# Optimization experiments

Hardware: AMD Instinct MI355X
Metric: run time of the kernel (lower is better)

The kernel has to match this reference:

```python
import jax, jax.numpy as jnp
import numpy as np

H_DIM = 64
GRID = 8
NBR = 2.0
BN_EPS = 1e-5
N_SEQ = 64
N_PED = 64
BOTTLENECK = 1024


def setup_inputs() -> dict:
    key = jax.random.key(0)
    k0, k1, k2, k3 = jax.random.split(key, 4)
    batch = N_SEQ * N_PED
    h_states = jax.random.normal(k0, (1, batch, H_DIM), jnp.float32)
    # positions spread over a 4x4 area so some neighbors fall inside the 2.0 neighborhood
    end_pos = jax.random.uniform(k1, (batch, 2), jnp.float32) * 4.0
    rel_pos = jax.random.normal(k2, (batch, 2), jnp.float32)
    starts = jnp.arange(N_SEQ, dtype=jnp.int32) * N_PED
    seq_start_end = jnp.stack([starts, starts + N_PED], axis=1)
    in_dim = GRID * GRID * H_DIM  # 4096
    W = jax.random.normal(k3, (in_dim, BOTTLENECK), jnp.float32) / np.sqrt(in_dim)
    b = jnp.zeros((BOTTLENECK,), jnp.float32)
    gamma = jnp.ones((BOTTLENECK,), jnp.float32)
    beta = jnp.zeros((BOTTLENECK,), jnp.float32)
    return {"h_states": h_states, "seq_start_end": seq_start_end, "end_pos": end_pos,
            "rel_pos": rel_pos, "W": W, "b": b, "gamma": gamma, "beta": beta}


def _pool_scene(hidden, pos):
    # hidden: (n, h), pos: (n, 2). Pair (i, j): ped j binned into ped i's grid.
    n, h = hidden.shape
    g2 = GRID * GRID
    half = NBR / 2.0
    tl_x = pos[:, 0] - half
    tl_y = pos[:, 1] + half
    br_x = pos[:, 0] + half
    br_y = pos[:, 1] - half
    px = pos[None, :, 0]  # (1, n) -> broadcast over i
    py = pos[None, :, 1]
    cell_x = jnp.floor((px - tl_x[:, None]) / NBR * GRID)
    cell_y = jnp.floor((tl_y[:, None] - py) / NBR * GRID)
    grid = (cell_x + cell_y * GRID).astype(jnp.int32) + 1  # slot 0 = trash bin
    oob = ((px >= br_x[:, None]) | (px <= tl_x[:, None]) |
           (py >= tl_y[:, None]) | (py <= br_y[:, None]) |
           jnp.eye(n, dtype=bool))  # self-interaction excluded
    grid = grid + (jnp.arange(n, dtype=jnp.int32) * g2)[:, None]
    grid = jnp.where(oob, 0, grid)  # (n, n)
    src = jnp.broadcast_to(hidden[None], (n, n, h)).reshape(-1, h)
    buf = jnp.zeros((n * g2 + 1, h), hidden.dtype).at[grid.reshape(-1)].add(src)
    return buf[1:].reshape(n, g2 * h)


def reference(h_states, seq_start_end, end_pos, rel_pos, W, b, gamma, beta):
    batch = end_pos.shape[0]
    n_seq = seq_start_end.shape[0]
    n_ped = batch // n_seq  # equal-length scenes by construction
    hid = h_states.reshape(-1, H_DIM).reshape(n_seq, n_ped, H_DIM)
    pos = end_pos.reshape(n_seq, n_ped, 2)
    pool_h = jax.vmap(_pool_scene)(hid, pos).reshape(batch, -1)  # (batch, 4096)
    x = pool_h @ W + b
    # BatchNorm1d in training mode (batch statistics, biased variance)
    mean = jnp.mean(x, axis=0)
    var = jnp.var(x, axis=0)
    x = (x - mean) * jax.lax.rsqrt(var + BN_EPS) * gamma + beta
    return jax.nn.relu(x)
```

## Files before the change

kernel.cpp:

```cpp
#include <hip/hip_runtime.h>
#include <hip/hip_bf16.h>


#define NPED  64
#define BATCH 4096
#define HDIM  64
#define G2    64
#define KDIM  4096
#define NOUT  1024

typedef __attribute__((ext_vector_type(8))) short short8;
typedef __attribute__((ext_vector_type(4))) float f32x4;

__device__ __forceinline__ unsigned short f2bf(float f) {
    __hip_bfloat16 h = __float2bfloat16(f);
    return *reinterpret_cast<unsigned short*>(&h);
}

__device__ __forceinline__ void lds_load16(const void* g, void* l) {
    __builtin_amdgcn_global_load_lds(
        (const __attribute__((address_space(1))) void*)g,
        (__attribute__((address_space(3))) void*)l, 16, 0, 0);
}

__global__ __launch_bounds__(512) void pool_kernel(const float* __restrict__ h,
                                                   const float* __restrict__ pos,
                                                   unsigned short* __restrict__ A2) {
    __shared__ float hs[NPED * HDIM];
    __shared__ float pl[NPED * 2];
    int t = threadIdx.x;
    int w = t >> 6, lane = t & 63;
    int p0 = blockIdx.x * 8;
    int sbase = p0 & ~(NPED - 1);
    if (t < 128) pl[t] = pos[sbase * 2 + t];
    {
        const float4* src = (const float4*)(h + (size_t)sbase * HDIM);
        float4* dst = (float4*)hs;
        dst[t] = src[t];
        dst[t + 512] = src[t + 512];
    }
    __syncthreads();

    int i = p0 + w;
    int il = i & (NPED - 1);
    float cx0 = pl[2 * il], cy0 = pl[2 * il + 1];
    float tlx = cx0 - 1.f, tly = cy0 + 1.f, brx = cx0 + 1.f, bry = cy0 - 1.f;
    float px = pl[2 * lane], py = pl[2 * lane + 1];
    bool inb = (lane != il) && !(px >= brx || px <= tlx || py >= tly || py <= bry);
    int cellx = (int)floorf((px - tlx) * 4.f);
    int celly = (int)floorf((tly - py) * 4.f);
    int cell = cellx + celly * 8;
    inb = inb && ((unsigned)cell < 64u);

    int mtile = i >> 4, r = i & 15;
    unsigned short* outb = A2 + (size_t)mtile * 65536 + r * 8
                              + (lane >> 5) * 512 + ((lane >> 3) & 3) * 128 + (lane & 7);
    const float* hrow = hs + lane;
    #pragma unroll
    for (int c = 0; c < 64; ++c) {
        unsigned long long m = __ballot(inb && (cell == c));
        float a = 0.f;
        while (m) {
            int j = __builtin_ctzll(m);
            m &= m - 1;
            a += hrow[j * HDIM];
        }
        outb[c * 1024] = f2bf(a);
    }
}

__global__ __launch_bounds__(256) void wt_kernel(const float* __restrict__ W,
                                                 unsigned short* __restrict__ Wt,
                                                 float* __restrict__ stats) {
    __shared__ unsigned short tile[64][66];
    int k0 = blockIdx.x * 64;
    int n0 = blockIdx.y * 64;
    int t = threadIdx.x;
    if (blockIdx.x == 0 && blockIdx.y < 8) stats[blockIdx.y * 256 + t] = 0.f;
    #pragma unroll
    for (int p = 0; p < 4; ++p) {
        int lin = p * 256 + t;
        int c4 = lin & 15, kl = lin >> 4;
        float4 v = ((const float4*)(W + (size_t)(k0 + kl) * NOUT + n0))[c4];
        tile[c4 * 4 + 0][kl] = f2bf(v.x);
        tile[c4 * 4 + 1][kl] = f2bf(v.y);
        tile[c4 * 4 + 2][kl] = f2bf(v.z);
        tile[c4 * 4 + 3][kl] = f2bf(v.w);
    }
    __syncthreads();
    unsigned int* out = (unsigned int*)Wt;
    #pragma unroll
    for (int p = 0; p < 8; ++p) {
        int lin = p * 256 + t;
        int ku = lin & 31, nl = lin >> 5;
        unsigned int v = (unsigned int)tile[nl][2 * ku] |
                         ((unsigned int)tile[nl][2 * ku + 1] << 16);
        out[(size_t)(n0 + nl) * (KDIM / 2) + (k0 >> 1) + ku] = v;
    }
}


__global__ __launch_bounds__(512, 2) void gemm_kernel(const unsigned short* __restrict__ A2,
                                                      const unsigned short* __restrict__ Bt,
                                                      float* __restrict__ C,
                                                      float* __restrict__ stats) {
    __shared__ __align__(16) char shmem[65536];
    unsigned short* Bs = (unsigned short*)shmem;

    int t = threadIdx.x;
    int w = t >> 6, lane = t & 63;
    int kh = w >> 2, wsub = w & 3;

    int bid = blockIdx.x;
    int yb = bid & 7, xb = bid >> 3;
    int m0 = xb * 128, n0 = yb * 128;
    int wm = (wsub >> 1) * 64, wn = (wsub & 1) * 64;

    const unsigned short* Ab = A2 + (size_t)((m0 >> 4) + (wm >> 4)) * 65536 + lane * 8;
    const unsigned short* Wtb = Bt + (size_t)n0 * KDIM;

    int kh_t = t >> 8, tt = t & 255;

    f32x4 acc[4][4];
    #pragma unroll
    for (int i = 0; i < 4; ++i)
        #pragma unroll
        for (int j = 0; j < 4; ++j)
            acc[i][j] = (f32x4){0.f, 0.f, 0.f, 0.f};

    for (int sk = 0; sk < 32; ++sk) {
        #pragma unroll
        for (int q = 0; q < 4; ++q) {
            int s = q * 256 + tt;
            int row = s >> 3;
            int swz = (s & 7) ^ (row & 7);
            lds_load16(Wtb + (size_t)row * KDIM + kh_t * 2048 + sk * 64 + swz * 8,
                       Bs + kh_t * 8192 + s * 8);
        }
        short8 af[2][4];
        #pragma unroll
        for (int kk = 0; kk < 2; ++kk)
            #pragma unroll
            for (int i = 0; i < 4; ++i)
                af[kk][i] = *(const short8*)(Ab + (size_t)i * 65536 +
                                             (size_t)(kh * 64 + sk * 2 + kk) * 512);
        __syncthreads();
        const unsigned short* Bsr = Bs + kh * 8192;
        #pragma unroll
        for (int kk = 0; kk < 2; ++kk) {
            #pragma unroll
            for (int j = 0; j < 4; ++j) {
                int rB = wn + j * 16 + (lane & 15);
                short8 b = *(const short8*)(Bsr + rB * 64 +
                               (((kk * 4 + (lane >> 4)) ^ (rB & 7)) * 8));
                #pragma unroll
                for (int i = 0; i < 4; ++i)
                    acc[i][j] = __builtin_amdgcn_mfma_f32_16x16x32_bf16(
                        af[kk][i], b, acc[i][j], 0, 0, 0);
            }
        }
        __syncthreads();
    }

    f32x4* red = (f32x4*)shmem;
    if (kh == 1) {
        #pragma unroll
        for (int i = 0; i < 4; ++i)
            #pragma unroll
            for (int j = 0; j < 4; ++j)
                red[(i * 4 + j) * 256 + tt] = acc[i][j];
    }
    __syncthreads();
    if (kh == 0) {
        #pragma unroll
        for (int i = 0; i < 4; ++i)
            #pragma unroll
            for (int j = 0; j < 4; ++j)
                acc[i][j] += red[(i * 4 + j) * 256 + t];

        int col0 = n0 + wn + (lane & 15);
        int row0 = m0 + wm + ((lane >> 4) << 2);
        #pragma unroll
        for (int j = 0; j < 4; ++j) {
            float s = 0.f, s2 = 0.f;
            #pragma unroll
            for (int i = 0; i < 4; ++i)
                #pragma unroll
                for (int r = 0; r < 4; ++r) {
                    float v = acc[i][j][r];
                    C[(size_t)(row0 + i * 16 + r) * NOUT + col0 + j * 16] = v;
                    s += v; s2 += v * v;
                }
            s  += __shfl_xor(s, 16);  s  += __shfl_xor(s, 32);
            s2 += __shfl_xor(s2, 16); s2 += __shfl_xor(s2, 32);
            if (lane < 16) {
                atomicAdd(&stats[col0 + j * 16], s);
                atomicAdd(&stats[NOUT + col0 + j * 16], s2);
            }
        }
    }
}

__global__ __launch_bounds__(256) void norm_kernel(float* __restrict__ C,
                                                   const float* __restrict__ stats,
                                                   const float* __restrict__ gamma,
                                                   const float* __restrict__ beta) {
    int idx = blockIdx.x * 256 + threadIdx.x;
    int col4 = idx & 255;
    float4 x = ((const float4*)C)[idx];
    float4 s = ((const float4*)stats)[col4];
    float4 q = ((const float4*)(stats + NOUT))[col4];
    float4 g = ((const float4*)gamma)[col4];
    float4 b = ((const float4*)beta)[col4];
    const float inv_n = 1.f / 4096.f;
    float m, inv;
    m = s.x * inv_n; inv = rsqrtf(q.x * inv_n - m * m + 1e-5f); x.x = fmaxf((x.x - m) * inv * g.x + b.x, 0.f);
    m = s.y * inv_n; inv = rsqrtf(q.y * inv_n - m * m + 1e-5f); x.y = fmaxf((x.y - m) * inv * g.y + b.y, 0.f);
    m = s.z * inv_n; inv = rsqrtf(q.z * inv_n - m * m + 1e-5f); x.z = fmaxf((x.z - m) * inv * g.z + b.z, 0.f);
    m = s.w * inv_n; inv = rsqrtf(q.w * inv_n - m * m + 1e-5f); x.w = fmaxf((x.w - m) * inv * g.w + b.w, 0.f);
    ((float4*)C)[idx] = x;
}

extern "C" void kernel_launch(void* const* d_in, const int* in_sizes, int n_in,
                              void* d_out, int out_size, void* d_ws, size_t ws_size,
                              hipStream_t stream) {
    const float* h      = (const float*)d_in[0];
    const float* endpos = (const float*)d_in[2];
    const float* W      = (const float*)d_in[4];
    const float* gamma  = (const float*)d_in[6];
    const float* beta   = (const float*)d_in[7];
    float* C = (float*)d_out;

    char* ws = (char*)d_ws;
    size_t off = 0;
    unsigned short* A2 = (unsigned short*)(ws + off); off += (size_t)BATCH * KDIM * 2;
    unsigned short* Wt = (unsigned short*)(ws + off); off += (size_t)NOUT * KDIM * 2;
    float* stats = (float*)(ws + off);

    pool_kernel<<<BATCH / 8, 512, 0, stream>>>(h, endpos, A2);
    wt_kernel<<<dim3(KDIM / 64, NOUT / 64), 256, 0, stream>>>(W, Wt, stats);
    gemm_kernel<<<dim3(256), 512, 0, stream>>>(A2, Wt, C, stats);
    norm_kernel<<<(BATCH * NOUT / 4) / 256, 256, 0, stream>>>(C, stats, gamma, beta);
}
```

Measured before the change: 164.1 us.

## Replace split-K GEMM with 64x128 tiles, 4 warps, no cross-warp reduction

Reworks the GEMM from 128x128 tiles with 8 waves splitting K into two halves (reduced through LDS) into 64x128 tiles with 4 waves, each covering all of K over 32 columns. The grid doubles to 512 blocks, and each iteration stages 128 K values of B into two LDS buffers. This removes the end-of-kernel split-K reduction and its extra LDS traffic, and gives more blocks for occupancy. In exchange, each wave does less MFMA work per B load, and A is re-read by twice as many blocks.

```diff
diff --git a/kernel.cpp b/kernel.cpp
--- a/kernel.cpp
+++ b/kernel.cpp
@@ -99,104 +99,80 @@
     }
 }
 
-
-__global__ __launch_bounds__(512, 2) void gemm_kernel(const unsigned short* __restrict__ A2,
+__global__ __launch_bounds__(256, 2) void gemm_kernel(const unsigned short* __restrict__ A2,
                                                       const unsigned short* __restrict__ Bt,
                                                       float* __restrict__ C,
                                                       float* __restrict__ stats) {
-    __shared__ __align__(16) char shmem[65536];
-    unsigned short* Bs = (unsigned short*)shmem;
-
+    __shared__ __align__(16) unsigned short Bs[2][128 * 64];
     int t = threadIdx.x;
     int w = t >> 6, lane = t & 63;
-    int kh = w >> 2, wsub = w & 3;
-
     int bid = blockIdx.x;
     int yb = bid & 7, xb = bid >> 3;
-    int m0 = xb * 128, n0 = yb * 128;
-    int wm = (wsub >> 1) * 64, wn = (wsub & 1) * 64;
-
-    const unsigned short* Ab = A2 + (size_t)((m0 >> 4) + (wm >> 4)) * 65536 + lane * 8;
-    const unsigned short* Wtb = Bt + (size_t)n0 * KDIM;
-
-    int kh_t = t >> 8, tt = t & 255;
-
-    f32x4 acc[4][4];
+    int m0 = xb * 64, n0 = yb * 128;
+    int wn = w * 32;
+
+    f32x4 acc[4][2];
     #pragma unroll
     for (int i = 0; i < 4; ++i)
         #pragma unroll
-        for (int j = 0; j < 4; ++j)
+        for (int j = 0; j < 2; ++j)
             acc[i][j] = (f32x4){0.f, 0.f, 0.f, 0.f};
 
-    for (int sk = 0; sk < 32; ++sk) {
+    int rbase = w * 32 + (lane >> 3);
+    int koff = ((lane & 7) ^ (lane >> 3)) * 8;
+    const unsigned short* Bg = Bt + (size_t)(n0 + rbase) * KDIM + koff;
+    unsigned short* BsW0 = &Bs[0][w * 2048 + lane * 8];
+    unsigned short* BsW1 = &Bs[1][w * 2048 + lane * 8];
+
+    const unsigned short* Abase = A2 + (size_t)(xb * 4) * 65536 + lane * 8;
+
+    for (int it = 0; it < 32; ++it) {
+        int kb = it * 128;
         #pragma unroll
         for (int q = 0; q < 4; ++q) {
-            int s = q * 256 + tt;
-            int row = s >> 3;
-            int swz = (s & 7) ^ (row & 7);
-            lds_load16(Wtb + (size_t)row * KDIM + kh_t * 2048 + sk * 64 + swz * 8,
-                       Bs + kh_t * 8192 + s * 8);
-        }
-        short8 af[2][4];
-        #pragma unroll
-        for (int kk = 0; kk < 2; ++kk)
+            lds_load16(Bg + (size_t)q * 8 * KDIM + kb,      BsW0 + q * 512);
+            lds_load16(Bg + (size_t)q * 8 * KDIM + kb + 64, BsW1 + q * 512);
+        }
+        short8 af[4][4];
+        #pragma unroll
+        for (int kk = 0; kk < 4; ++kk)
             #pragma unroll
             for (int i = 0; i < 4; ++i)
-                af[kk][i] = *(const short8*)(Ab + (size_t)i * 65536 +
-                                             (size_t)(kh * 64 + sk * 2 + kk) * 512);
+                af[kk][i] = *(const short8*)(Abase + ((size_t)i * 128 + it * 4 + kk) * 512);
         __syncthreads();
-        const unsigned short* Bsr = Bs + kh * 8192;
-        #pragma unroll
-        for (int kk = 0; kk < 2; ++kk) {
+        #pragma unroll
+        for (int kk = 0; kk < 4; ++kk) {
+            const unsigned short* Bsr = Bs[kk >> 1];
+            int chunk = (((kk & 1) * 4 + (lane >> 4)) ^ (lane & 7)) * 8;
             #pragma unroll
-            for (int j = 0; j < 4; ++j) {
-                int rB = wn + j * 16 + (lane & 15);
-                short8 b = *(const short8*)(Bsr + rB * 64 +
-                               (((kk * 4 + (lane >> 4)) ^ (rB & 7)) * 8));
+            for (int j = 0; j < 2; ++j) {
+                short8 b = *(const short8*)&Bsr[(wn + j * 16 + (lane & 15)) * 64 + chunk];
                 #pragma unroll
                 for (int i = 0; i < 4; ++i)
-                    acc[i][j] = __builtin_amdgcn_mfma_f32_16x16x32_bf16(
-                        af[kk][i], b, acc[i][j], 0, 0, 0);
+                    acc[i][j] = __builtin_amdgcn_mfma_f32_16x16x32_bf16(af[kk][i], b, acc[i][j], 0, 0, 0);
             }
         }
         __syncthreads();
     }
 
-    f32x4* red = (f32x4*)shmem;
-    if (kh == 1) {
+    int col0 = n0 + wn + (lane & 15);
+    int row0 = m0 + ((lane >> 4) << 2);
+    #pragma unroll
+    for (int j = 0; j < 2; ++j) {
+        float s = 0.f, s2 = 0.f;
         #pragma unroll
         for (int i = 0; i < 4; ++i)
             #pragma unroll
-            for (int j = 0; j < 4; ++j)
-                red[(i * 4 + j) * 256 + tt] = acc[i][j];
-    }
-    __syncthreads();
-    if (kh == 0) {
-        #pragma unroll
-        for (int i = 0; i < 4; ++i)
-            #pragma unroll
-            for (int j = 0; j < 4; ++j)
-                acc[i][j] += red[(i * 4 + j) * 256 + t];
-
-        int col0 = n0 + wn + (lane & 15);
-        int row0 = m0 + wm + ((lane >> 4) << 2);
-        #pragma unroll
-        for (int j = 0; j < 4; ++j) {
-            float s = 0.f, s2 = 0.f;
-            #pragma unroll
-            for (int i = 0; i < 4; ++i)
-                #pragma unroll
-                for (int r = 0; r < 4; ++r) {
-                    float v = acc[i][j][r];
-                    C[(size_t)(row0 + i * 16 + r) * NOUT + col0 + j * 16] = v;
-                    s += v; s2 += v * v;
-                }
-            s  += __shfl_xor(s, 16);  s  += __shfl_xor(s, 32);
-            s2 += __shfl_xor(s2, 16); s2 += __shfl_xor(s2, 32);
-            if (lane < 16) {
-                atomicAdd(&stats[col0 + j * 16], s);
-                atomicAdd(&stats[NOUT + col0 + j * 16], s2);
+            for (int r = 0; r < 4; ++r) {
+                float v = acc[i][j][r];
+                C[(size_t)(row0 + i * 16 + r) * NOUT + col0 + j * 16] = v;
+                s += v; s2 += v * v;
             }
+        s  += __shfl_xor(s, 16);  s  += __shfl_xor(s, 32);
+        s2 += __shfl_xor(s2, 16); s2 += __shfl_xor(s2, 32);
+        if (lane < 16) {
+            atomicAdd(&stats[col0 + j * 16], s);
+            atomicAdd(&stats[NOUT + col0 + j * 16], s2);
         }
     }
 }
@@ -239,6 +215,6 @@
 
     pool_kernel<<<BATCH / 8, 512, 0, stream>>>(h, endpos, A2);
     wt_kernel<<<dim3(KDIM / 64, NOUT / 64), 256, 0, stream>>>(W, Wt, stats);
-    gemm_kernel<<<dim3(256), 512, 0, stream>>>(A2, Wt, C, stats);
+    gemm_kernel<<<dim3(512), 256, 0, stream>>>(A2, Wt, C, stats);
     norm_kernel<<<(BATCH * NOUT / 4) / 256, 256, 0, stream>>>(C, stats, gamma, beta);
 }
```

Result: no change. 167.1 us (+1.9%).
